# Optimization experiments

Measured on AMD Instinct MI355X. Metric: run time of the kernel, lower is better.

The kernel has to match this reference:

```python
import jax, jax.numpy as jnp
import numpy as np
from jax.scipy.linalg import expm

N_WIRES = 9
N_LAYERS = 4
EMBED = 512
BATCH = 64
D = 2 ** N_WIRES
P = N_WIRES * N_LAYERS * 2  # gate angles per sample


def _apply_gate(st, g, w):
    # st: (D, 2,...,2) complex64; apply 2x2 gate g on wire w
    st = jnp.moveaxis(st, 1 + w, -1)
    st = st @ g.T  # new[a] = sum_b g[a,b] old[b]
    return jnp.moveaxis(st, -1, 1 + w)


def _apply_cnot(st, c, t):
    st = jnp.moveaxis(st, (1 + c, 1 + t), (-2, -1))
    st = jnp.concatenate([st[..., 0:1, :], st[..., 1:2, ::-1]], axis=-2)
    return jnp.moveaxis(st, (-2, -1), (1 + c, 1 + t))


def _build_unitary(params):
    # simulate circuit on all D basis states at once (identity input)
    st = jnp.eye(D, dtype=jnp.complex64).reshape((D,) + (2,) * N_WIRES)
    idx = 0
    for _ in range(N_LAYERS):
        for w in range(N_WIRES):
            thy = params[idx]
            thz = params[idx + 1]
            idx += 2
            c = jnp.cos(thy * 0.5).astype(jnp.complex64)
            s = jnp.sin(thy * 0.5).astype(jnp.complex64)
            ry = jnp.stack([jnp.stack([c, -s]), jnp.stack([s, c])])
            ep = jnp.exp(0.5j * thz.astype(jnp.complex64))  # exp(i*thz/2)
            zero = jnp.zeros((), jnp.complex64)
            rz = jnp.stack([jnp.stack([jnp.conj(ep), zero]), jnp.stack([zero, ep])])
            st = _apply_gate(st, rz @ ry, w)  # Ry then Rz, fused
        for w in range(N_WIRES - 1):
            st = _apply_cnot(st, w, w + 1)
        st = _apply_cnot(st, N_WIRES - 1, 0)  # ring entangler (n_wires>1)
    # row index = input basis state i -> column i of U; take real part
    return jnp.real(st.reshape(D, D)).T


def _forward(t, w1, b1, w2, b2):
    h = jax.nn.silu(t[:, None] @ w1 + b1)          # (B, EMBED)
    params = h @ w2 + b2                            # (B, P)
    p_sg = jax.lax.stop_gradient(params)            # torch uses .detach() for the circuit
    U_stack = jax.vmap(_build_unitary)(p_sg)        # (B, D, D)
    B = t.shape[0]
    A = jnp.zeros((B, D * D), params.dtype).at[:, :P].set(params).reshape(B, D, D)
    A_skew = (A - jnp.swapaxes(A, -1, -2)) * 0.01
    U_diff = jax.vmap(expm)(A_skew)                 # (B, D, D)
    return jnp.einsum('bij,bjk->bik', U_stack, U_diff)


def setup_inputs() -> dict:
    key = jax.random.key(0)
    k_t, k1, kb1, k2, kb2 = jax.random.split(key, 5)
    t = jax.random.normal(k_t, (BATCH,), jnp.float32)
    w1 = jax.random.normal(k1, (1, EMBED), jnp.float32)
    b1 = jax.random.normal(kb1, (EMBED,), jnp.float32) * 0.1
    w2 = jax.random.normal(k2, (EMBED, P), jnp.float32) / np.sqrt(EMBED)
    b2 = jax.random.normal(kb2, (P,), jnp.float32) * 0.1
    return {"t": t, "w1": w1, "b1": b1, "w2": w2, "b2": b2}


def reference(t, w1, b1, w2, b2):
    return _forward(t, w1, b1, w2, b2)
```

## Files before the change

### kernel.cpp

```cpp
#include <hip/hip_runtime.h>
#include <math.h>


#define PSTRIDE 2560
#define GD_OFF  0
#define SC_OFF  144
#define L_OFF(l) (160 + (l)*256)
#define V_OFF   1184
#define W_OFF   1280
#define C0_OFF  1792

__device__ __forceinline__ float2 cmul(float2 a, float2 b){
  return make_float2(fmaf(a.x, b.x, -a.y*b.y), fmaf(a.x, b.y, a.y*b.x));
}

__device__ __forceinline__ float2 pk_fma_s_lo(float2 s2, float2 b, float2 c){
  float2 d;
  asm("v_pk_fma_f32 %0, %1, %2, %3 op_sel:[0,0,0] op_sel_hi:[0,1,1]"
      : "=v"(d) : "s"(s2), "v"(b), "v"(c));
  return d;
}
__device__ __forceinline__ float2 pk_mul_s_hi(float2 s2, float2 b){
  float2 d;
  asm("v_pk_mul_f32 %0, %1, %2 op_sel:[1,0] op_sel_hi:[1,1]"
      : "=v"(d) : "s"(s2), "v"(b));
  return d;
}
__device__ __forceinline__ float2 pk_fma_vs_lo(float2 a, float2 b, float2 c){
  float2 d;
  asm("v_pk_fma_f32 %0, %1, %2, %3 op_sel:[0,0,0] op_sel_hi:[0,1,1]"
      : "=v"(d) : "v"(a), "s"(b), "v"(c));
  return d;
}
__device__ __forceinline__ float2 pk_mul_vs_hi(float2 a, float2 b){
  float2 d;
  asm("v_pk_mul_f32 %0, %1, %2 op_sel:[1,0] op_sel_hi:[1,1]"
      : "=v"(d) : "v"(a), "s"(b));
  return d;
}
__device__ __forceinline__ float2 pk_fma_vv_lo(float2 a, float2 b, float2 c){
  float2 d;
  asm("v_pk_fma_f32 %0, %1, %2, %3 op_sel:[0,0,0] op_sel_hi:[0,1,1]"
      : "=v"(d) : "v"(a), "v"(b), "v"(c));
  return d;
}
__device__ __forceinline__ float2 pk_mul_vv_hi(float2 a, float2 b){
  float2 d;
  asm("v_pk_mul_f32 %0, %1, %2 op_sel:[1,0] op_sel_hi:[1,1]"
      : "=v"(d) : "v"(a), "v"(b));
  return d;
}
__device__ __forceinline__ float2 pk_swapneg(float2 c, float2 n){
  float2 d;
  asm("v_pk_mul_f32 %0, %1, %2 op_sel:[1,0] op_sel_hi:[0,1]"
      : "=v"(d) : "v"(c), "v"(n));
  return d;
}

__device__ __forceinline__ float2 f4lo(float4 v){ return make_float2(v.x, v.y); }
__device__ __forceinline__ float2 f4hi(float4 v){ return make_float2(v.z, v.w); }
__device__ __forceinline__ float4 mk4(float2 a, float2 b){
  float4 r; r.x = a.x; r.y = a.y; r.z = b.x; r.w = b.y; return r;
}

__device__ __forceinline__ int Fperm(int x){
  int S = x ^ (x >> 1); S ^= S >> 2; S ^= S >> 4; S ^= S >> 8;
  return (S & 0xFF) | ((((x >> 8) ^ S) & 1) << 8);
}
__device__ __forceinline__ int physmap(int x){ return x ^ ((x >> 4) & 15); }

template<int STRIDE>
__device__ __forceinline__ void apply_rot2(float2 amp[8], const float* rp){
  const float2 R0 = ((const float2*)rp)[0];
  const float2 R1 = ((const float2*)rp)[1];
  #pragma unroll
  for (int b = 0; b < 8; ++b){
    if (b & STRIDE) continue;
    const float2 u = amp[b], v = amp[b + STRIDE];
    amp[b]          = pk_fma_vv_lo(R0, u, pk_mul_vv_hi(R0, v));
    amp[b + STRIDE] = pk_fma_vv_lo(R1, u, pk_mul_vv_hi(R1, v));
  }
}

__device__ __forceinline__ void run_layer2(float2* __restrict__ S,
    const float* __restrict__ lb, const int lane,
    const int base1, const int base2, const int base3, const int baseF,
    const float2 NEG1P1){
  float2 amp[8];
  #pragma unroll
  for (int j = 0; j < 8; ++j) amp[j] = S[base1 ^ j];
  apply_rot2<4>(amp, lb + 6*4);
  apply_rot2<2>(amp, lb + 7*4);
  apply_rot2<1>(amp, lb + 8*4);
  #pragma unroll
  for (int j = 0; j < 8; ++j) S[base1 ^ j] = amp[j];
  #pragma unroll
  for (int j = 0; j < 8; ++j) amp[j] = S[base2 ^ ((j << 3) ^ (j >> 1))];
  apply_rot2<4>(amp, lb + 3*4);
  apply_rot2<2>(amp, lb + 4*4);
  apply_rot2<1>(amp, lb + 5*4);
  #pragma unroll
  for (int j = 0; j < 8; ++j) S[base2 ^ ((j << 3) ^ (j >> 1))] = amp[j];
  #pragma unroll
  for (int j = 0; j < 8; ++j) amp[j] = S[base3 ^ ((j << 6) ^ ((4*j) & 15))];
  apply_rot2<4>(amp, lb + 0*4);
  apply_rot2<2>(amp, lb + 1*4);
  apply_rot2<1>(amp, lb + 2*4);
  {
    const float2 A  = *(const float2*)(lb + 128 + lane*2);
    const float2 A2 = pk_swapneg(A, NEG1P1);
    #pragma unroll
    for (int j = 0; j < 8; ++j)
      amp[j] = pk_fma_vv_lo(amp[j], A, pk_mul_vv_hi(amp[j], A2));
    #pragma unroll
    for (int j = 0; j < 8; ++j){
      const float2 P = *(const float2*)(lb + 64 + j*4);
      const float2 Q = *(const float2*)(lb + 64 + j*4 + 2);
      amp[j] = pk_fma_vv_lo(amp[j], P, pk_mul_vv_hi(amp[j], Q));
    }
  }
  #pragma unroll
  for (int j = 0; j < 8; ++j) S[baseF ^ physmap(Fperm(j << 6))] = amp[j];
}

template<int STRIDE>
__device__ __forceinline__ void apply_rot4(float4 amp[8], const float* rp){
  const float2 R0 = ((const float2*)rp)[0];
  const float2 R1 = ((const float2*)rp)[1];
  #pragma unroll
  for (int b = 0; b < 8; ++b){
    if (b & STRIDE) continue;
    const float2 ulo = f4lo(amp[b]),        uhi = f4hi(amp[b]);
    const float2 vlo = f4lo(amp[b+STRIDE]), vhi = f4hi(amp[b+STRIDE]);
    amp[b]          = mk4(pk_fma_s_lo(R0, ulo, pk_mul_s_hi(R0, vlo)),
                          pk_fma_s_lo(R0, uhi, pk_mul_s_hi(R0, vhi)));
    amp[b + STRIDE] = mk4(pk_fma_s_lo(R1, ulo, pk_mul_s_hi(R1, vlo)),
                          pk_fma_s_lo(R1, uhi, pk_mul_s_hi(R1, vhi)));
  }
}

__device__ __forceinline__ void run_layer4(float4* __restrict__ S,
    const float* __restrict__ lb, const int lane,
    const int base1, const int base2, const int base3, const int baseF,
    const float2 NEG1P1){
  float4 amp[8];
  #pragma unroll
  for (int j = 0; j < 8; ++j) amp[j] = S[base1 ^ j];
  apply_rot4<4>(amp, lb + 6*4);
  apply_rot4<2>(amp, lb + 7*4);
  apply_rot4<1>(amp, lb + 8*4);
  #pragma unroll
  for (int j = 0; j < 8; ++j) S[base1 ^ j] = amp[j];
  #pragma unroll
  for (int j = 0; j < 8; ++j) amp[j] = S[base2 ^ ((j << 3) ^ (j >> 1))];
  apply_rot4<4>(amp, lb + 3*4);
  apply_rot4<2>(amp, lb + 4*4);
  apply_rot4<1>(amp, lb + 5*4);
  #pragma unroll
  for (int j = 0; j < 8; ++j) S[base2 ^ ((j << 3) ^ (j >> 1))] = amp[j];
  #pragma unroll
  for (int j = 0; j < 8; ++j) amp[j] = S[base3 ^ ((j << 6) ^ ((4*j) & 15))];
  apply_rot4<4>(amp, lb + 0*4);
  apply_rot4<2>(amp, lb + 1*4);
  apply_rot4<1>(amp, lb + 2*4);
  {
    const float2 A  = *(const float2*)(lb + 128 + lane*2);
    const float2 A2 = pk_swapneg(A, NEG1P1);
    #pragma unroll
    for (int j = 0; j < 8; ++j){
      const float2 lo = f4lo(amp[j]), hi = f4hi(amp[j]);
      amp[j] = mk4(pk_fma_vv_lo(lo, A, pk_mul_vv_hi(lo, A2)),
                   pk_fma_vv_lo(hi, A, pk_mul_vv_hi(hi, A2)));
    }
    #pragma unroll
    for (int j = 0; j < 8; ++j){
      const float2 P = *(const float2*)(lb + 64 + j*4);
      const float2 Q = *(const float2*)(lb + 64 + j*4 + 2);
      const float2 lo = f4lo(amp[j]), hi = f4hi(amp[j]);
      amp[j] = mk4(pk_fma_vs_lo(lo, P, pk_mul_vs_hi(lo, Q)),
                   pk_fma_vs_lo(hi, P, pk_mul_vs_hi(hi, Q)));
    }
  }
  #pragma unroll
  for (int j = 0; j < 8; ++j) S[baseF ^ physmap(Fperm(j << 6))] = amp[j];
}

__global__ __launch_bounds__(576)
void prep_kernel(const float* __restrict__ t,  const float* __restrict__ w1,
                 const float* __restrict__ b1, const float* __restrict__ w2,
                 const float* __restrict__ b2, float* __restrict__ prep){
  __shared__ float sh[512];
  __shared__ float part[8][72];
  __shared__ float spar[72];
  __shared__ float tl[4][256];
  __shared__ float ssc[3];
  __shared__ __align__(16) float2 vst[2][512];
  const int s = blockIdx.x;
  const float ts = t[s];
  for (int k = threadIdx.x; k < 512; k += 576){
    const float z = fmaf(ts, w1[k], b1[k]);
    sh[k] = z / (1.f + expf(-z));
  }
  __syncthreads();
  {
    const int p = threadIdx.x % 72, c = threadIdx.x / 72;
    float acc = 0.f;
    const int k0 = c*64;
    for (int k = k0; k < k0 + 64; ++k) acc = fmaf(sh[k], w2[k*72 + p], acc);
    part[c][p] = acc;
  }
  __syncthreads();
  if (threadIdx.x < 72){
    const int p = threadIdx.x;
    float acc = b2[p];
    #pragma unroll
    for (int c = 0; c < 8; ++c) acc += part[c][p];
    spar[p] = acc;
  }
  __syncthreads();
  float* pb = prep + (size_t)s*PSTRIDE;
  const int tid = threadIdx.x;
  if (tid < 256){
    const int l = tid >> 6, m = tid & 63;
    float2 acc = make_float2(1.f, 0.f);
    #pragma unroll
    for (int w = 3; w < 9; ++w){
      const float thz = spar[2*(9*l + w) + 1];
      float zi, zr; sincosf(0.5f*thz, &zi, &zr);
      const int bit = (m >> (8 - w)) & 1;
      acc = cmul(acc, make_float2(zr, bit ? zi : -zi));
    }
    pb[L_OFF(l) + 128 + 2*m]     = acc.x;
    pb[L_OFF(l) + 128 + 2*m + 1] = acc.y;
    tl[l][128 + 2*m]     = acc.x;
    tl[l][128 + 2*m + 1] = acc.y;
  } else if (tid < 288){
    const int q = tid - 256, l = q >> 3, j = q & 7;
    float2 acc = make_float2(1.f, 0.f);
    #pragma unroll
    for (int w = 0; w < 3; ++w){
      const float thz = spar[2*(9*l + w) + 1];
      float zi, zr; sincosf(0.5f*thz, &zi, &zr);
      const int bit = (j >> (2 - w)) & 1;
      acc = cmul(acc, make_float2(zr, bit ? zi : -zi));
    }
    float* o = pb + L_OFF(l) + 64 + j*4;
    o[0] = acc.x; o[1] = acc.y; o[2] = -acc.y; o[3] = acc.x;
    float* o2 = &tl[l][64 + j*4];
    o2[0] = acc.x; o2[1] = acc.y; o2[2] = -acc.y; o2[3] = acc.x;
  } else if (tid < 324){
    const int q = tid - 288, l = q / 9, w = q - l*9;
    const float thy = spar[2*(9*l + w)];
    float sy, cy; sincosf(0.5f*thy, &sy, &cy);
    float* o = pb + L_OFF(l) + w*4;
    o[0] = cy; o[1] = -sy; o[2] = sy; o[3] = cy;
    float* o2 = &tl[l][w*4];
    o2[0] = cy; o2[1] = -sy; o2[2] = sy; o2[3] = cy;
  } else if (tid < 333){
    const int w = tid - 324;
    const float thy = spar[2*w], thz = spar[2*w + 1];
    float sy, cy, zi, zr;
    sincosf(0.5f*thy, &sy, &cy);
    sincosf(0.5f*thz, &zi, &zr);
    const float gr[4] = { zr*cy, -zr*sy, zr*sy, zr*cy };
    const float gi[4] = { -zi*cy, zi*sy, zi*sy, zi*cy };
    float* o = pb + GD_OFF + w*16;
    #pragma unroll
    for (int e = 0; e < 4; ++e){
      o[e*4+0] = gr[e]; o[e*4+1] = gi[e]; o[e*4+2] = -gi[e]; o[e*4+3] = gr[e];
    }
  } else if (tid < 405){
    const int j = tid - 333;
    pb[V_OFF + j] = (j == 0) ? 0.f : 0.01f*spar[j];
  } else if (tid == 405){
    float th2 = 0.f;
    for (int j = 1; j < 72; ++j){ const float v = 0.01f*spar[j]; th2 = fmaf(v, v, th2); }
    const float th = sqrtf(th2);
    float alpha, beta;
    if (th > 1e-6f){
      alpha = sinf(th)/th;
      const float s2 = sinf(0.5f*th);
      beta = 2.f*s2*s2/th2;
    } else { alpha = 1.f - th2/6.f; beta = 0.5f; }
    pb[SC_OFF+0] = cosf(th);
    pb[SC_OFF+1] = alpha;
    pb[SC_OFF+2] = beta;
    ssc[0] = cosf(th); ssc[1] = alpha; ssc[2] = beta;
  }
  __syncthreads();
  if (tid < 128){
    const int wv = tid >> 6, lane = tid & 63;
    float2* const S = vst[wv];
    const float2 NEG1P1 = make_float2(-1.f, 1.f);
    const int base1 = (lane << 3) ^ ((lane >> 1) & 15);
    const int hq = lane >> 3, lq = lane & 7;
    const int base2 = (hq << 6) ^ ((hq << 2) & 15) ^ lq;
    const int base3 = lane ^ (lane >> 4);
    const int baseF = physmap(Fperm(lane));
    #pragma unroll
    for (int j = 0; j < 8; ++j){
      const int x = (lane << 3) + j;
      float re;
      if (wv == 0) re = (x == 0) ? 1.f : 0.f;
      else         re = (x >= 1 && x < 72) ? 0.01f*spar[x] : 0.f;
      S[base1 ^ j] = make_float2(re, 0.f);
    }
    #pragma unroll
    for (int L = 0; L < 4; ++L)
      run_layer2(S, &tl[L][0], lane, base1, base2, base3, baseF, NEG1P1);
  }
  __syncthreads();
  if (tid < 512){
    const int a  = tid;
    const int pa = a ^ ((a >> 4) & 15);
    const float u0 = vst[0][pa].x;
    const float uv = vst[1][pa].x;
    pb[W_OFF  + a] = fmaf(ssc[1], u0, -ssc[2]*uv);
    pb[C0_OFF + a] = fmaf(ssc[0], u0, -ssc[1]*uv);
  }
}

__global__ __launch_bounds__(256, 6)
void sim_kernel(const float* __restrict__ prep, float* __restrict__ out){
  __shared__ __align__(16) float4 st[4][512];
  const int s    = blockIdx.x & 63;
  const int cb   = blockIdx.x >> 6;
  const int wid  = threadIdx.x >> 6;
  const int lane = threadIdx.x & 63;
  const float* gp = prep + (size_t)s*PSTRIDE;
  float4* const S = st[wid];
  const float2 NEG1P1 = make_float2(-1.f, 1.f);

  float4 amp[8];
  {
    float2 base = make_float2(1.f, 0.f);
    #pragma unroll
    for (int w = 0; w < 6; ++w){
      const int xb = (lane >> (5 - w)) & 1;
      const int ib = (cb   >> (5 - w)) & 1;
      const float4 gd = *(const float4*)(gp + GD_OFF + w*16 + (xb*2 + ib)*4);
      const float2 d1 = make_float2(gd.x, gd.y);
      const float2 d2 = make_float2(gd.z, gd.w);
      base = pk_fma_vv_lo(base, d1, pk_mul_vv_hi(base, d2));
    }
    const int i6 = (wid >> 1) & 1, i7 = wid & 1;
    float2 g6[2], g7[2];
    float4 g8d[4];
    #pragma unroll
    for (int r = 0; r < 2; ++r){
      g6[r]      = *(const float2*)(gp + GD_OFF + 6*16 + (r*2 + i6)*4);
      g7[r]      = *(const float2*)(gp + GD_OFF + 7*16 + (r*2 + i7)*4);
      g8d[r*2+0] = *(const float4*)(gp + GD_OFF + 8*16 + (r*2 + 0)*4);
      g8d[r*2+1] = *(const float4*)(gp + GD_OFF + 8*16 + (r*2 + 1)*4);
    }
    float2 g67[4];
    #pragma unroll
    for (int a = 0; a < 2; ++a)
      #pragma unroll
      for (int b = 0; b < 2; ++b)
        g67[a*2+b] = cmul(g6[a], g7[b]);
    const float2 bd2 = pk_swapneg(base, NEG1P1);
    #pragma unroll
    for (int j = 0; j < 8; ++j){
      const float2 T  = g67[j >> 1];
      const float4 ga = g8d[(j & 1)*2 + 0];
      const float4 gb = g8d[(j & 1)*2 + 1];
      const float2 Ta = pk_fma_vv_lo(T, make_float2(ga.x, ga.y),
                                     pk_mul_vv_hi(T, make_float2(ga.z, ga.w)));
      const float2 Tb = pk_fma_vv_lo(T, make_float2(gb.x, gb.y),
                                     pk_mul_vv_hi(T, make_float2(gb.z, gb.w)));
      amp[j] = mk4(pk_fma_vv_lo(Ta, base, pk_mul_vv_hi(Ta, bd2)),
                   pk_fma_vv_lo(Tb, base, pk_mul_vv_hi(Tb, bd2)));
    }
    const int bFI = physmap(Fperm(lane << 3));
    #pragma unroll
    for (int j = 0; j < 8; ++j) S[bFI ^ physmap(Fperm(j))] = amp[j];
  }

  const int base1 = (lane << 3) ^ ((lane >> 1) & 15);
  const int hq = lane >> 3, lq = lane & 7;
  const int base2 = (hq << 6) ^ ((hq << 2) & 15) ^ lq;
  const int base3 = lane ^ (lane >> 4);
  const int baseF = physmap(Fperm(lane));

  run_layer4(S, gp + L_OFF(1), lane, base1, base2, base3, baseF, NEG1P1);
  run_layer4(S, gp + L_OFF(2), lane, base1, base2, base3, baseF, NEG1P1);
  run_layer4(S, gp + L_OFF(3), lane, base1, base2, base3, baseF, NEG1P1);

  __syncthreads();
  const float* wt  = gp + W_OFF;
  const float* c0t = gp + C0_OFF;
  const float* vt  = gp + V_OFF;
  const int q  = threadIdx.x & 1;
  const int a0 = threadIdx.x >> 1;
  #pragma unroll
  for (int rep = 0; rep < 4; ++rep){
    const int a  = a0 + rep*128;
    const int pa = a ^ ((a >> 4) & 15);
    float4 vv;
    vv.x = st[q*2 + 0][pa].x;
    vv.y = st[q*2 + 0][pa].z;
    vv.z = st[q*2 + 1][pa].x;
    vv.w = st[q*2 + 1][pa].z;
    if (cb < 9){
      const float  wa = wt[a];
      const float4 vj = *(const float4*)(vt + cb*8 + q*4);
      vv.x = fmaf(wa, vj.x, vv.x);
      vv.y = fmaf(wa, vj.y, vv.y);
      vv.z = fmaf(wa, vj.z, vv.z);
      vv.w = fmaf(wa, vj.w, vv.w);
      if ((cb | q) == 0) vv.x = c0t[a];
    }
    *(float4*)&out[(size_t)s*262144 + (size_t)a*512 + cb*8 + q*4] = vv;
  }
}

extern "C" void kernel_launch(void* const* d_in, const int* in_sizes, int n_in,
                              void* d_out, int out_size, void* d_ws, size_t ws_size,
                              hipStream_t stream){
  const float* t  = (const float*)d_in[0];
  const float* w1 = (const float*)d_in[1];
  const float* b1 = (const float*)d_in[2];
  const float* w2 = (const float*)d_in[3];
  const float* b2 = (const float*)d_in[4];
  float* out  = (float*)d_out;
  float* prep = (float*)d_ws;
  prep_kernel<<<64,   576, 0, stream>>>(t, w1, b1, w2, b2, prep);
  sim_kernel <<<4096, 256, 0, stream>>>(prep, out);
}
```

Before: 145.2 us.

## Halve sim block to two waves and split LDS float4 stores

The simulation kernel moves from 4096 blocks of four wavefronts to 8192 blocks of two wavefronts. Each block now covers 4 output columns instead of 8, and the column-bit indexing is remapped to match. Amplitudes are held as pairs of float2, and LDS stores are written as two 8-byte writes instead of one 16-byte write, probably to ease register pressure or bank conflicts. The smaller blocks are meant to improve scheduling and occupancy, at the cost of narrower 16-byte output segments per block and more launch and setup overhead.

```diff
diff --git a/kernel.cpp b/kernel.cpp
--- a/kernel.cpp
+++ b/kernel.cpp
@@ -57,12 +57,6 @@
   return d;
 }
 
-__device__ __forceinline__ float2 f4lo(float4 v){ return make_float2(v.x, v.y); }
-__device__ __forceinline__ float2 f4hi(float4 v){ return make_float2(v.z, v.w); }
-__device__ __forceinline__ float4 mk4(float2 a, float2 b){
-  float4 r; r.x = a.x; r.y = a.y; r.z = b.x; r.w = b.y; return r;
-}
-
 __device__ __forceinline__ int Fperm(int x){
   int S = x ^ (x >> 1); S ^= S >> 2; S ^= S >> 4; S ^= S >> 8;
   return (S & 0xFF) | ((((x >> 8) ^ S) & 1) << 8);
@@ -123,66 +117,76 @@
   for (int j = 0; j < 8; ++j) S[baseF ^ physmap(Fperm(j << 6))] = amp[j];
 }
 
+struct camp { float2 lo, hi; };
+
+__device__ __forceinline__ camp lds_ld(const float4* S, int idx){
+  const float4 v = S[idx];
+  camp a; a.lo = make_float2(v.x, v.y); a.hi = make_float2(v.z, v.w);
+  return a;
+}
+__device__ __forceinline__ void lds_st(float4* S, int idx, camp a){
+  float2* p = (float2*)(S + idx);
+  p[0] = a.lo; p[1] = a.hi;
+}
+
 template<int STRIDE>
-__device__ __forceinline__ void apply_rot4(float4 amp[8], const float* rp){
+__device__ __forceinline__ void apply_rotc(camp amp[8], const float* rp){
   const float2 R0 = ((const float2*)rp)[0];
   const float2 R1 = ((const float2*)rp)[1];
   #pragma unroll
   for (int b = 0; b < 8; ++b){
     if (b & STRIDE) continue;
-    const float2 ulo = f4lo(amp[b]),        uhi = f4hi(amp[b]);
-    const float2 vlo = f4lo(amp[b+STRIDE]), vhi = f4hi(amp[b+STRIDE]);
-    amp[b]          = mk4(pk_fma_s_lo(R0, ulo, pk_mul_s_hi(R0, vlo)),
-                          pk_fma_s_lo(R0, uhi, pk_mul_s_hi(R0, vhi)));
-    amp[b + STRIDE] = mk4(pk_fma_s_lo(R1, ulo, pk_mul_s_hi(R1, vlo)),
-                          pk_fma_s_lo(R1, uhi, pk_mul_s_hi(R1, vhi)));
-  }
-}
-
-__device__ __forceinline__ void run_layer4(float4* __restrict__ S,
+    const float2 ul = amp[b].lo,        uh = amp[b].hi;
+    const float2 vl = amp[b+STRIDE].lo, vh = amp[b+STRIDE].hi;
+    amp[b].lo        = pk_fma_s_lo(R0, ul, pk_mul_s_hi(R0, vl));
+    amp[b].hi        = pk_fma_s_lo(R0, uh, pk_mul_s_hi(R0, vh));
+    amp[b+STRIDE].lo = pk_fma_s_lo(R1, ul, pk_mul_s_hi(R1, vl));
+    amp[b+STRIDE].hi = pk_fma_s_lo(R1, uh, pk_mul_s_hi(R1, vh));
+  }
+}
+
+__device__ __forceinline__ void run_layerc(float4* __restrict__ S,
     const float* __restrict__ lb, const int lane,
     const int base1, const int base2, const int base3, const int baseF,
     const float2 NEG1P1){
-  float4 amp[8];
-  #pragma unroll
-  for (int j = 0; j < 8; ++j) amp[j] = S[base1 ^ j];
-  apply_rot4<4>(amp, lb + 6*4);
-  apply_rot4<2>(amp, lb + 7*4);
-  apply_rot4<1>(amp, lb + 8*4);
-  #pragma unroll
-  for (int j = 0; j < 8; ++j) S[base1 ^ j] = amp[j];
-  #pragma unroll
-  for (int j = 0; j < 8; ++j) amp[j] = S[base2 ^ ((j << 3) ^ (j >> 1))];
-  apply_rot4<4>(amp, lb + 3*4);
-  apply_rot4<2>(amp, lb + 4*4);
-  apply_rot4<1>(amp, lb + 5*4);
-  #pragma unroll
-  for (int j = 0; j < 8; ++j) S[base2 ^ ((j << 3) ^ (j >> 1))] = amp[j];
-  #pragma unroll
-  for (int j = 0; j < 8; ++j) amp[j] = S[base3 ^ ((j << 6) ^ ((4*j) & 15))];
-  apply_rot4<4>(amp, lb + 0*4);
-  apply_rot4<2>(amp, lb + 1*4);
-  apply_rot4<1>(amp, lb + 2*4);
+  camp amp[8];
+  #pragma unroll
+  for (int j = 0; j < 8; ++j) amp[j] = lds_ld(S, base1 ^ j);
+  apply_rotc<4>(amp, lb + 6*4);
+  apply_rotc<2>(amp, lb + 7*4);
+  apply_rotc<1>(amp, lb + 8*4);
+  #pragma unroll
+  for (int j = 0; j < 8; ++j) lds_st(S, base1 ^ j, amp[j]);
+  #pragma unroll
+  for (int j = 0; j < 8; ++j) amp[j] = lds_ld(S, base2 ^ ((j << 3) ^ (j >> 1)));
+  apply_rotc<4>(amp, lb + 3*4);
+  apply_rotc<2>(amp, lb + 4*4);
+  apply_rotc<1>(amp, lb + 5*4);
+  #pragma unroll
+  for (int j = 0; j < 8; ++j) lds_st(S, base2 ^ ((j << 3) ^ (j >> 1)), amp[j]);
+  #pragma unroll
+  for (int j = 0; j < 8; ++j) amp[j] = lds_ld(S, base3 ^ ((j << 6) ^ ((4*j) & 15)));
+  apply_rotc<4>(amp, lb + 0*4);
+  apply_rotc<2>(amp, lb + 1*4);
+  apply_rotc<1>(amp, lb + 2*4);
   {
     const float2 A  = *(const float2*)(lb + 128 + lane*2);
     const float2 A2 = pk_swapneg(A, NEG1P1);
     #pragma unroll
     for (int j = 0; j < 8; ++j){
-      const float2 lo = f4lo(amp[j]), hi = f4hi(amp[j]);
-      amp[j] = mk4(pk_fma_vv_lo(lo, A, pk_mul_vv_hi(lo, A2)),
-                   pk_fma_vv_lo(hi, A, pk_mul_vv_hi(hi, A2)));
+      amp[j].lo = pk_fma_vv_lo(amp[j].lo, A, pk_mul_vv_hi(amp[j].lo, A2));
+      amp[j].hi = pk_fma_vv_lo(amp[j].hi, A, pk_mul_vv_hi(amp[j].hi, A2));
     }
     #pragma unroll
     for (int j = 0; j < 8; ++j){
       const float2 P = *(const float2*)(lb + 64 + j*4);
       const float2 Q = *(const float2*)(lb + 64 + j*4 + 2);
-      const float2 lo = f4lo(amp[j]), hi = f4hi(amp[j]);
-      amp[j] = mk4(pk_fma_vs_lo(lo, P, pk_mul_vs_hi(lo, Q)),
-                   pk_fma_vs_lo(hi, P, pk_mul_vs_hi(hi, Q)));
-    }
-  }
-  #pragma unroll
-  for (int j = 0; j < 8; ++j) S[baseF ^ physmap(Fperm(j << 6))] = amp[j];
+      amp[j].lo = pk_fma_vs_lo(amp[j].lo, P, pk_mul_vs_hi(amp[j].lo, Q));
+      amp[j].hi = pk_fma_vs_lo(amp[j].hi, P, pk_mul_vs_hi(amp[j].hi, Q));
+    }
+  }
+  #pragma unroll
+  for (int j = 0; j < 8; ++j) lds_st(S, baseF ^ physmap(Fperm(j << 6)), amp[j]);
 }
 
 __global__ __launch_bounds__(576)
@@ -320,9 +324,9 @@
   }
 }
 
-__global__ __launch_bounds__(256, 6)
+__global__ __launch_bounds__(128, 5)
 void sim_kernel(const float* __restrict__ prep, float* __restrict__ out){
-  __shared__ __align__(16) float4 st[4][512];
+  __shared__ __align__(16) float4 st[2][512];
   const int s    = blockIdx.x & 63;
   const int cb   = blockIdx.x >> 6;
   const int wid  = threadIdx.x >> 6;
@@ -331,19 +335,19 @@
   float4* const S = st[wid];
   const float2 NEG1P1 = make_float2(-1.f, 1.f);
 
-  float4 amp[8];
+  camp amp[8];
   {
     float2 base = make_float2(1.f, 0.f);
     #pragma unroll
     for (int w = 0; w < 6; ++w){
       const int xb = (lane >> (5 - w)) & 1;
-      const int ib = (cb   >> (5 - w)) & 1;
+      const int ib = (cb   >> (6 - w)) & 1;
       const float4 gd = *(const float4*)(gp + GD_OFF + w*16 + (xb*2 + ib)*4);
       const float2 d1 = make_float2(gd.x, gd.y);
       const float2 d2 = make_float2(gd.z, gd.w);
       base = pk_fma_vv_lo(base, d1, pk_mul_vv_hi(base, d2));
     }
-    const int i6 = (wid >> 1) & 1, i7 = wid & 1;
+    const int i6 = cb & 1, i7 = wid & 1;
     float2 g6[2], g7[2];
     float4 g8d[4];
     #pragma unroll
@@ -369,12 +373,12 @@
                                      pk_mul_vv_hi(T, make_float2(ga.z, ga.w)));
       const float2 Tb = pk_fma_vv_lo(T, make_float2(gb.x, gb.y),
                                      pk_mul_vv_hi(T, make_float2(gb.z, gb.w)));
-      amp[j] = mk4(pk_fma_vv_lo(Ta, base, pk_mul_vv_hi(Ta, bd2)),
-                   pk_fma_vv_lo(Tb, base, pk_mul_vv_hi(Tb, bd2)));
+      amp[j].lo = pk_fma_vv_lo(Ta, base, pk_mul_vv_hi(Ta, bd2));
+      amp[j].hi = pk_fma_vv_lo(Tb, base, pk_mul_vv_hi(Tb, bd2));
     }
     const int bFI = physmap(Fperm(lane << 3));
     #pragma unroll
-    for (int j = 0; j < 8; ++j) S[bFI ^ physmap(Fperm(j))] = amp[j];
+    for (int j = 0; j < 8; ++j) lds_st(S, bFI ^ physmap(Fperm(j)), amp[j]);
   }
 
   const int base1 = (lane << 3) ^ ((lane >> 1) & 15);
@@ -383,35 +387,32 @@
   const int base3 = lane ^ (lane >> 4);
   const int baseF = physmap(Fperm(lane));
 
-  run_layer4(S, gp + L_OFF(1), lane, base1, base2, base3, baseF, NEG1P1);
-  run_layer4(S, gp + L_OFF(2), lane, base1, base2, base3, baseF, NEG1P1);
-  run_layer4(S, gp + L_OFF(3), lane, base1, base2, base3, baseF, NEG1P1);
+  run_layerc(S, gp + L_OFF(1), lane, base1, base2, base3, baseF, NEG1P1);
+  run_layerc(S, gp + L_OFF(2), lane, base1, base2, base3, baseF, NEG1P1);
+  run_layerc(S, gp + L_OFF(3), lane, base1, base2, base3, baseF, NEG1P1);
 
   __syncthreads();
   const float* wt  = gp + W_OFF;
   const float* c0t = gp + C0_OFF;
   const float* vt  = gp + V_OFF;
-  const int q  = threadIdx.x & 1;
-  const int a0 = threadIdx.x >> 1;
   #pragma unroll
   for (int rep = 0; rep < 4; ++rep){
-    const int a  = a0 + rep*128;
+    const int a  = threadIdx.x + rep*128;
     const int pa = a ^ ((a >> 4) & 15);
+    const float4 w0 = st[0][pa];
+    const float4 w1 = st[1][pa];
     float4 vv;
-    vv.x = st[q*2 + 0][pa].x;
-    vv.y = st[q*2 + 0][pa].z;
-    vv.z = st[q*2 + 1][pa].x;
-    vv.w = st[q*2 + 1][pa].z;
-    if (cb < 9){
+    vv.x = w0.x; vv.y = w0.z; vv.z = w1.x; vv.w = w1.z;
+    if (cb < 18){
       const float  wa = wt[a];
-      const float4 vj = *(const float4*)(vt + cb*8 + q*4);
+      const float4 vj = *(const float4*)(vt + cb*4);
       vv.x = fmaf(wa, vj.x, vv.x);
       vv.y = fmaf(wa, vj.y, vv.y);
       vv.z = fmaf(wa, vj.z, vv.z);
       vv.w = fmaf(wa, vj.w, vv.w);
-      if ((cb | q) == 0) vv.x = c0t[a];
-    }
-    *(float4*)&out[(size_t)s*262144 + (size_t)a*512 + cb*8 + q*4] = vv;
+      if (cb == 0) vv.x = c0t[a];
+    }
+    *(float4*)&out[(size_t)s*262144 + (size_t)a*512 + cb*4] = vv;
   }
 }
 
@@ -426,5 +427,5 @@
   float* out  = (float*)d_out;
   float* prep = (float*)d_ws;
   prep_kernel<<<64,   576, 0, stream>>>(t, w1, b1, w2, b2, prep);
-  sim_kernel <<<4096, 256, 0, stream>>>(prep, out);
-}
+  sim_kernel <<<8192, 128, 0, stream>>>(prep, out);
+}
```

Measured after the change: 153.1 us. 5.5% more time.

## Restructure circuit simulation so each 16-lane group holds 32 amplitudes per column

Applied to the files above, without the earlier changes.

The sim kernel now uses 128-thread blocks. Each 16-lane group simulates one output column and keeps 32 complex amplitudes in registers, replacing the old scheme of 64 lanes with 8 float4 amplitudes covering two columns each. Gate layers now take two shared-memory passes (5+4 wires) instead of three (3+3+3), and the prep kernel recomputes the diagonal phase tables into a new 32/16 split. This cuts shared-memory round trips per layer but raises register pressure (32 float2 per thread) and changes occupancy, via launch bounds 128,2 and smaller blocks.

```diff
diff --git a/kernel.cpp b/kernel.cpp
--- a/kernel.cpp
+++ b/kernel.cpp
@@ -57,17 +57,12 @@
   return d;
 }
 
-__device__ __forceinline__ float2 f4lo(float4 v){ return make_float2(v.x, v.y); }
-__device__ __forceinline__ float2 f4hi(float4 v){ return make_float2(v.z, v.w); }
-__device__ __forceinline__ float4 mk4(float2 a, float2 b){
-  float4 r; r.x = a.x; r.y = a.y; r.z = b.x; r.w = b.y; return r;
-}
-
 __device__ __forceinline__ int Fperm(int x){
   int S = x ^ (x >> 1); S ^= S >> 2; S ^= S >> 4; S ^= S >> 8;
   return (S & 0xFF) | ((((x >> 8) ^ S) & 1) << 8);
 }
 __device__ __forceinline__ int physmap(int x){ return x ^ ((x >> 4) & 15); }
+__device__ __forceinline__ int pm2(int y){ return y ^ (((y >> 5) & 15) << 1); }
 
 template<int STRIDE>
 __device__ __forceinline__ void apply_rot2(float2 amp[8], const float* rp){
@@ -124,65 +119,16 @@
 }
 
 template<int STRIDE>
-__device__ __forceinline__ void apply_rot4(float4 amp[8], const float* rp){
+__device__ __forceinline__ void rot32(float2 amp[32], const float* rp){
   const float2 R0 = ((const float2*)rp)[0];
   const float2 R1 = ((const float2*)rp)[1];
   #pragma unroll
-  for (int b = 0; b < 8; ++b){
+  for (int b = 0; b < 32; ++b){
     if (b & STRIDE) continue;
-    const float2 ulo = f4lo(amp[b]),        uhi = f4hi(amp[b]);
-    const float2 vlo = f4lo(amp[b+STRIDE]), vhi = f4hi(amp[b+STRIDE]);
-    amp[b]          = mk4(pk_fma_s_lo(R0, ulo, pk_mul_s_hi(R0, vlo)),
-                          pk_fma_s_lo(R0, uhi, pk_mul_s_hi(R0, vhi)));
-    amp[b + STRIDE] = mk4(pk_fma_s_lo(R1, ulo, pk_mul_s_hi(R1, vlo)),
-                          pk_fma_s_lo(R1, uhi, pk_mul_s_hi(R1, vhi)));
-  }
-}
-
-__device__ __forceinline__ void run_layer4(float4* __restrict__ S,
-    const float* __restrict__ lb, const int lane,
-    const int base1, const int base2, const int base3, const int baseF,
-    const float2 NEG1P1){
-  float4 amp[8];
-  #pragma unroll
-  for (int j = 0; j < 8; ++j) amp[j] = S[base1 ^ j];
-  apply_rot4<4>(amp, lb + 6*4);
-  apply_rot4<2>(amp, lb + 7*4);
-  apply_rot4<1>(amp, lb + 8*4);
-  #pragma unroll
-  for (int j = 0; j < 8; ++j) S[base1 ^ j] = amp[j];
-  #pragma unroll
-  for (int j = 0; j < 8; ++j) amp[j] = S[base2 ^ ((j << 3) ^ (j >> 1))];
-  apply_rot4<4>(amp, lb + 3*4);
-  apply_rot4<2>(amp, lb + 4*4);
-  apply_rot4<1>(amp, lb + 5*4);
-  #pragma unroll
-  for (int j = 0; j < 8; ++j) S[base2 ^ ((j << 3) ^ (j >> 1))] = amp[j];
-  #pragma unroll
-  for (int j = 0; j < 8; ++j) amp[j] = S[base3 ^ ((j << 6) ^ ((4*j) & 15))];
-  apply_rot4<4>(amp, lb + 0*4);
-  apply_rot4<2>(amp, lb + 1*4);
-  apply_rot4<1>(amp, lb + 2*4);
-  {
-    const float2 A  = *(const float2*)(lb + 128 + lane*2);
-    const float2 A2 = pk_swapneg(A, NEG1P1);
-    #pragma unroll
-    for (int j = 0; j < 8; ++j){
-      const float2 lo = f4lo(amp[j]), hi = f4hi(amp[j]);
-      amp[j] = mk4(pk_fma_vv_lo(lo, A, pk_mul_vv_hi(lo, A2)),
-                   pk_fma_vv_lo(hi, A, pk_mul_vv_hi(hi, A2)));
-    }
-    #pragma unroll
-    for (int j = 0; j < 8; ++j){
-      const float2 P = *(const float2*)(lb + 64 + j*4);
-      const float2 Q = *(const float2*)(lb + 64 + j*4 + 2);
-      const float2 lo = f4lo(amp[j]), hi = f4hi(amp[j]);
-      amp[j] = mk4(pk_fma_vs_lo(lo, P, pk_mul_vs_hi(lo, Q)),
-                   pk_fma_vs_lo(hi, P, pk_mul_vs_hi(hi, Q)));
-    }
-  }
-  #pragma unroll
-  for (int j = 0; j < 8; ++j) S[baseF ^ physmap(Fperm(j << 6))] = amp[j];
+    const float2 u = amp[b], v = amp[b + STRIDE];
+    amp[b]          = pk_fma_s_lo(R0, u, pk_mul_s_hi(R0, v));
+    amp[b + STRIDE] = pk_fma_s_lo(R1, u, pk_mul_s_hi(R1, v));
+  }
 }
 
 __global__ __launch_bounds__(576)
@@ -230,8 +176,6 @@
       const int bit = (m >> (8 - w)) & 1;
       acc = cmul(acc, make_float2(zr, bit ? zi : -zi));
     }
-    pb[L_OFF(l) + 128 + 2*m]     = acc.x;
-    pb[L_OFF(l) + 128 + 2*m + 1] = acc.y;
     tl[l][128 + 2*m]     = acc.x;
     tl[l][128 + 2*m + 1] = acc.y;
   } else if (tid < 288){
@@ -244,8 +188,6 @@
       const int bit = (j >> (2 - w)) & 1;
       acc = cmul(acc, make_float2(zr, bit ? zi : -zi));
     }
-    float* o = pb + L_OFF(l) + 64 + j*4;
-    o[0] = acc.x; o[1] = acc.y; o[2] = -acc.y; o[3] = acc.x;
     float* o2 = &tl[l][64 + j*4];
     o2[0] = acc.x; o2[1] = acc.y; o2[2] = -acc.y; o2[3] = acc.x;
   } else if (tid < 324){
@@ -286,6 +228,36 @@
     pb[SC_OFF+1] = alpha;
     pb[SC_OFF+2] = beta;
     ssc[0] = cosf(th); ssc[1] = alpha; ssc[2] = beta;
+  } else if (tid < 502){
+    const int q = tid - 406, l = (q >> 5) + 1, i = q & 31;
+    float2 acc = make_float2(1.f, 0.f);
+    float zi, zr;
+    sincosf(0.5f*spar[2*(9*l + 0) + 1], &zi, &zr);
+    acc = cmul(acc, make_float2(zr, ((i >> 4) & 1) ? zi : -zi));
+    sincosf(0.5f*spar[2*(9*l + 1) + 1], &zi, &zr);
+    acc = cmul(acc, make_float2(zr, ((i >> 3) & 1) ? zi : -zi));
+    sincosf(0.5f*spar[2*(9*l + 2) + 1], &zi, &zr);
+    acc = cmul(acc, make_float2(zr, ((i >> 2) & 1) ? zi : -zi));
+    sincosf(0.5f*spar[2*(9*l + 3) + 1], &zi, &zr);
+    acc = cmul(acc, make_float2(zr, ((i >> 1) & 1) ? zi : -zi));
+    sincosf(0.5f*spar[2*(9*l + 8) + 1], &zi, &zr);
+    acc = cmul(acc, make_float2(zr, (i & 1) ? zi : -zi));
+    float* o = pb + L_OFF(l) + 64 + i*4;
+    o[0] = acc.x; o[1] = acc.y; o[2] = -acc.y; o[3] = acc.x;
+  } else if (tid < 550){
+    const int q = tid - 502, l = (q >> 4) + 1, m = q & 15;
+    float2 acc = make_float2(1.f, 0.f);
+    float zi, zr;
+    sincosf(0.5f*spar[2*(9*l + 4) + 1], &zi, &zr);
+    acc = cmul(acc, make_float2(zr, ((m >> 3) & 1) ? zi : -zi));
+    sincosf(0.5f*spar[2*(9*l + 5) + 1], &zi, &zr);
+    acc = cmul(acc, make_float2(zr, ((m >> 2) & 1) ? zi : -zi));
+    sincosf(0.5f*spar[2*(9*l + 6) + 1], &zi, &zr);
+    acc = cmul(acc, make_float2(zr, ((m >> 1) & 1) ? zi : -zi));
+    sincosf(0.5f*spar[2*(9*l + 7) + 1], &zi, &zr);
+    acc = cmul(acc, make_float2(zr, (m & 1) ? zi : -zi));
+    pb[L_OFF(l) + 192 + m*2]     = acc.x;
+    pb[L_OFF(l) + 192 + m*2 + 1] = acc.y;
   }
   __syncthreads();
   if (tid < 128){
@@ -320,72 +292,114 @@
   }
 }
 
-__global__ __launch_bounds__(256, 6)
+__global__ __launch_bounds__(128, 2)
 void sim_kernel(const float* __restrict__ prep, float* __restrict__ out){
-  __shared__ __align__(16) float4 st[4][512];
+  __shared__ __align__(16) float2 ST[2][2048];
   const int s    = blockIdx.x & 63;
   const int cb   = blockIdx.x >> 6;
   const int wid  = threadIdx.x >> 6;
   const int lane = threadIdx.x & 63;
+  const int g    = lane >> 4;
+  const int mu   = lane & 15;
+  const int col  = cb*8 + wid*4 + g;
   const float* gp = prep + (size_t)s*PSTRIDE;
-  float4* const S = st[wid];
-  const float2 NEG1P1 = make_float2(-1.f, 1.f);
-
-  float4 amp[8];
+  float2* const S = ST[wid];
+  const int Wbase = g*512;
+  const int tm    = 2*mu;
+  const int rdb   = Wbase + mu*32;
+
+  float2 amp[32];
   {
     float2 base = make_float2(1.f, 0.f);
     #pragma unroll
-    for (int w = 0; w < 6; ++w){
-      const int xb = (lane >> (5 - w)) & 1;
-      const int ib = (cb   >> (5 - w)) & 1;
-      const float4 gd = *(const float4*)(gp + GD_OFF + w*16 + (xb*2 + ib)*4);
-      const float2 d1 = make_float2(gd.x, gd.y);
-      const float2 d2 = make_float2(gd.z, gd.w);
-      base = pk_fma_vv_lo(base, d1, pk_mul_vv_hi(base, d2));
-    }
-    const int i6 = (wid >> 1) & 1, i7 = wid & 1;
-    float2 g6[2], g7[2];
-    float4 g8d[4];
-    #pragma unroll
-    for (int r = 0; r < 2; ++r){
-      g6[r]      = *(const float2*)(gp + GD_OFF + 6*16 + (r*2 + i6)*4);
-      g7[r]      = *(const float2*)(gp + GD_OFF + 7*16 + (r*2 + i7)*4);
-      g8d[r*2+0] = *(const float4*)(gp + GD_OFF + 8*16 + (r*2 + 0)*4);
-      g8d[r*2+1] = *(const float4*)(gp + GD_OFF + 8*16 + (r*2 + 1)*4);
-    }
-    float2 g67[4];
-    #pragma unroll
-    for (int a = 0; a < 2; ++a)
+    for (int w = 0; w < 4; ++w){
+      const int xb = (mu  >> (3 - w)) & 1;
+      const int ib = (col >> (8 - w)) & 1;
+      const float2 gv = *(const float2*)(gp + GD_OFF + w*16 + (xb*2 + ib)*4);
+      base = cmul(base, gv);
+    }
+    float2 a4[2], a5[2], a6[2], a7[2], a8[2];
+    #pragma unroll
+    for (int b = 0; b < 2; ++b){
+      a4[b] = *(const float2*)(gp + GD_OFF + 4*16 + (b*2 + ((col>>4)&1))*4);
+      a5[b] = *(const float2*)(gp + GD_OFF + 5*16 + (b*2 + ((col>>3)&1))*4);
+      a6[b] = *(const float2*)(gp + GD_OFF + 6*16 + (b*2 + ((col>>2)&1))*4);
+      a7[b] = *(const float2*)(gp + GD_OFF + 7*16 + (b*2 + ((col>>1)&1))*4);
+      a8[b] = *(const float2*)(gp + GD_OFF + 8*16 + (b*2 + (col&1))*4);
+    }
+    float2 t1[2], t2[4], t3[8], t4[16];
+    #pragma unroll
+    for (int b = 0; b < 2; ++b) t1[b] = cmul(base, a4[b]);
+    #pragma unroll
+    for (int k = 0; k < 2; ++k)
       #pragma unroll
-      for (int b = 0; b < 2; ++b)
-        g67[a*2+b] = cmul(g6[a], g7[b]);
-    const float2 bd2 = pk_swapneg(base, NEG1P1);
-    #pragma unroll
-    for (int j = 0; j < 8; ++j){
-      const float2 T  = g67[j >> 1];
-      const float4 ga = g8d[(j & 1)*2 + 0];
-      const float4 gb = g8d[(j & 1)*2 + 1];
-      const float2 Ta = pk_fma_vv_lo(T, make_float2(ga.x, ga.y),
-                                     pk_mul_vv_hi(T, make_float2(ga.z, ga.w)));
-      const float2 Tb = pk_fma_vv_lo(T, make_float2(gb.x, gb.y),
-                                     pk_mul_vv_hi(T, make_float2(gb.z, gb.w)));
-      amp[j] = mk4(pk_fma_vv_lo(Ta, base, pk_mul_vv_hi(Ta, bd2)),
-                   pk_fma_vv_lo(Tb, base, pk_mul_vv_hi(Tb, bd2)));
-    }
-    const int bFI = physmap(Fperm(lane << 3));
-    #pragma unroll
-    for (int j = 0; j < 8; ++j) S[bFI ^ physmap(Fperm(j))] = amp[j];
-  }
-
-  const int base1 = (lane << 3) ^ ((lane >> 1) & 15);
-  const int hq = lane >> 3, lq = lane & 7;
-  const int base2 = (hq << 6) ^ ((hq << 2) & 15) ^ lq;
-  const int base3 = lane ^ (lane >> 4);
-  const int baseF = physmap(Fperm(lane));
-
-  run_layer4(S, gp + L_OFF(1), lane, base1, base2, base3, baseF, NEG1P1);
-  run_layer4(S, gp + L_OFF(2), lane, base1, base2, base3, baseF, NEG1P1);
-  run_layer4(S, gp + L_OFF(3), lane, base1, base2, base3, baseF, NEG1P1);
+      for (int b = 0; b < 2; ++b) t2[k*2+b] = cmul(t1[k], a5[b]);
+    #pragma unroll
+    for (int k = 0; k < 4; ++k)
+      #pragma unroll
+      for (int b = 0; b < 2; ++b) t3[k*2+b] = cmul(t2[k], a6[b]);
+    #pragma unroll
+    for (int k = 0; k < 8; ++k)
+      #pragma unroll
+      for (int b = 0; b < 2; ++b) t4[k*2+b] = cmul(t3[k], a7[b]);
+    #pragma unroll
+    for (int i = 0; i < 32; ++i) amp[i] = cmul(t4[i>>1], a8[i&1]);
+    const int IbB = Wbase + pm2(Fperm(mu << 5));
+    #pragma unroll
+    for (int i = 0; i < 32; ++i) S[IbB ^ pm2(Fperm(i))] = amp[i];
+  }
+
+  const int Fb2 = Wbase + pm2(Fperm(mu << 1));
+  const float2 NEG1P1 = make_float2(-1.f, 1.f);
+
+  #pragma unroll
+  for (int L = 1; L <= 3; ++L){
+    const float* lb = gp + L_OFF(L);
+    #pragma unroll
+    for (int a = 0; a < 16; ++a){
+      const float4 v = *(const float4*)&S[rdb + ((2*a) ^ tm)];
+      amp[2*a]   = make_float2(v.x, v.y);
+      amp[2*a+1] = make_float2(v.z, v.w);
+    }
+    rot32<16>(amp, lb + 4*4);
+    rot32< 8>(amp, lb + 5*4);
+    rot32< 4>(amp, lb + 6*4);
+    rot32< 2>(amp, lb + 7*4);
+    rot32< 1>(amp, lb + 8*4);
+    #pragma unroll
+    for (int a = 0; a < 16; ++a){
+      const int sl = Wbase + a*32 + (tm ^ ((2*a) & 31));
+      float4 v; v.x = amp[2*a].x; v.y = amp[2*a].y;
+      v.z = amp[2*a+1].x; v.w = amp[2*a+1].y;
+      *(float4*)&S[sl] = v;
+    }
+    #pragma unroll
+    for (int a = 0; a < 16; ++a){
+      const float4 v = *(const float4*)&S[rdb + ((2*a) ^ tm)];
+      amp[2*a]   = make_float2(v.x, v.y);
+      amp[2*a+1] = make_float2(v.z, v.w);
+    }
+    rot32<16>(amp, lb + 0*4);
+    rot32< 8>(amp, lb + 1*4);
+    rot32< 4>(amp, lb + 2*4);
+    rot32< 2>(amp, lb + 3*4);
+    {
+      const float2 A  = *(const float2*)(lb + 192 + mu*2);
+      const float2 A2 = pk_swapneg(A, NEG1P1);
+      #pragma unroll
+      for (int i = 0; i < 32; ++i)
+        amp[i] = pk_fma_vv_lo(amp[i], A, pk_mul_vv_hi(amp[i], A2));
+      #pragma unroll
+      for (int i = 0; i < 32; ++i){
+        const float2 P = *(const float2*)(lb + 64 + i*4);
+        const float2 Q = *(const float2*)(lb + 64 + i*4 + 2);
+        amp[i] = pk_fma_vs_lo(amp[i], P, pk_mul_vs_hi(amp[i], Q));
+      }
+    }
+    #pragma unroll
+    for (int i = 0; i < 32; ++i)
+      S[Fb2 ^ pm2(Fperm(((i >> 1) << 5) | (i & 1)))] = amp[i];
+  }
 
   __syncthreads();
   const float* wt  = gp + W_OFF;
@@ -394,24 +408,24 @@
   const int q  = threadIdx.x & 1;
   const int a0 = threadIdx.x >> 1;
   #pragma unroll
-  for (int rep = 0; rep < 4; ++rep){
-    const int a  = a0 + rep*128;
-    const int pa = a ^ ((a >> 4) & 15);
+  for (int rep = 0; rep < 8; ++rep){
+    const int r  = a0 + rep*64;
+    const int pr = pm2(r);
     float4 vv;
-    vv.x = st[q*2 + 0][pa].x;
-    vv.y = st[q*2 + 0][pa].z;
-    vv.z = st[q*2 + 1][pa].x;
-    vv.w = st[q*2 + 1][pa].z;
+    vv.x = ST[q][0*512 + pr].x;
+    vv.y = ST[q][1*512 + pr].x;
+    vv.z = ST[q][2*512 + pr].x;
+    vv.w = ST[q][3*512 + pr].x;
     if (cb < 9){
-      const float  wa = wt[a];
+      const float  wa = wt[r];
       const float4 vj = *(const float4*)(vt + cb*8 + q*4);
       vv.x = fmaf(wa, vj.x, vv.x);
       vv.y = fmaf(wa, vj.y, vv.y);
       vv.z = fmaf(wa, vj.z, vv.z);
       vv.w = fmaf(wa, vj.w, vv.w);
-      if ((cb | q) == 0) vv.x = c0t[a];
-    }
-    *(float4*)&out[(size_t)s*262144 + (size_t)a*512 + cb*8 + q*4] = vv;
+      if ((cb | q) == 0) vv.x = c0t[r];
+    }
+    *(float4*)&out[(size_t)s*262144 + (size_t)r*512 + cb*8 + q*4] = vv;
   }
 }
 
@@ -426,5 +440,5 @@
   float* out  = (float*)d_out;
   float* prep = (float*)d_ws;
   prep_kernel<<<64,   576, 0, stream>>>(t, w1, b1, w2, b2, prep);
-  sim_kernel <<<4096, 256, 0, stream>>>(prep, out);
-}
+  sim_kernel <<<4096, 128, 0, stream>>>(prep, out);
+}
```

Measured after the change: 160.7 us. 10.7% more time.
